# Kernel tuning notes

Measured on AMD Instinct MI355X. Metric: run time of the kernel, lower is better.

## Reference

```python
import jax
jax.config.update("jax_enable_x64", True)
import jax.numpy as jnp
import numpy as np
import math

B, L = 4, 4096
VOCAB, CVOCAB = 32000, 25000
HIDDEN, EDIM, NHEADS = 1024, 64, 8
NGRAMS = (2, 3)
TABLE_HINT = 100003
KSIZE, DILATION = 4, 3  # dilation = max ngram order
EPS = 1e-6


def _next_prime(n):
    if n <= 2:
        return 2
    c = n if n % 2 else n + 1
    while True:
        if all(c % i for i in range(3, int(math.isqrt(c)) + 1, 2)):
            return c
        c += 2


def _table_sizes():
    sizes, cur = [], TABLE_HINT
    for _ in range(NHEADS):
        p = _next_prime(cur)
        sizes.append(p)
        cur = p + 2
    return sizes


def setup_inputs():
    key = jax.random.key(0)
    ks = jax.random.split(key, 12)
    sizes = _table_sizes()  # identical for both ngram orders (same hint)
    max_s = max(sizes)
    n_orders = NGRAMS[1] - NGRAMS[0] + 1  # 2
    table_sizes = jnp.asarray(np.tile(np.array(sizes, dtype=np.int64), (n_orders, 1)))  # [2,8]
    tables = 0.01 * jax.random.normal(ks[0], (n_orders, NHEADS, max_s, EDIM), dtype=jnp.float32)
    return {
        "hidden_states": jax.random.normal(ks[1], (B, L, HIDDEN), dtype=jnp.float32),
        "token_ids": jax.random.randint(ks[2], (B, L), 0, VOCAB, dtype=jnp.int64),
        "projection": jax.random.randint(ks[3], (VOCAB,), 0, CVOCAB, dtype=jnp.int64),
        "mults2": jax.random.randint(ks[4], (NHEADS, 2), 1, 2**31 - 1, dtype=jnp.int64),
        "mults3": jax.random.randint(ks[5], (NHEADS, 3), 1, 2**31 - 1, dtype=jnp.int64),
        "table_sizes": table_sizes,
        "tables": tables,
        "w_k": (jax.random.normal(ks[6], (HIDDEN, n_orders * NHEADS * EDIM), dtype=jnp.float32) / math.sqrt(n_orders * NHEADS * EDIM)),
        "w_v": (jax.random.normal(ks[7], (HIDDEN, n_orders * NHEADS * EDIM), dtype=jnp.float32) / math.sqrt(n_orders * NHEADS * EDIM)),
        "q_norm_w": jnp.ones((HIDDEN,), dtype=jnp.float32),
        "k_norm_w": jnp.ones((HIDDEN,), dtype=jnp.float32),
        "conv_norm_w": jnp.ones((HIDDEN,), dtype=jnp.float32),
        "conv_w": 0.02 * jax.random.normal(ks[8], (HIDDEN, KSIZE), dtype=jnp.float32),
        "conv_b": jnp.zeros((HIDDEN,), dtype=jnp.float32),
    }


def _rmsnorm(x, w):
    norm = jax.lax.rsqrt(jnp.mean(jnp.square(x.astype(jnp.float32)), axis=-1, keepdims=True) + EPS)
    return (x.astype(jnp.float32) * norm).astype(x.dtype) * w


def _build_ngrams(compressed, n):
    # compressed: [B,L] int64 -> [B,L,n] causal windows with left zero pad
    p = jnp.pad(compressed, ((0, 0), (n - 1, 0)))
    return jnp.stack([p[:, i:i + compressed.shape[1]] for i in range(n)], axis=-1)


def _hash(ngrams, mults, sizes):
    # ngrams [B,L,n], mults [H,n], sizes [H] -> [B,L,H]
    prod = ngrams[:, :, None, :] * mults[None, None, :, :]  # int64
    mix = prod[..., 0]
    for i in range(1, prod.shape[-1]):
        mix = mix ^ prod[..., i]
    return jnp.abs(mix) % sizes[None, None, :]


def reference(hidden_states, token_ids, projection, mults2, mults3, table_sizes,
              tables, w_k, w_v, q_norm_w, k_norm_w, conv_norm_w, conv_w, conv_b):
    b, l, hidden = hidden_states.shape
    # ---- retrieve ----
    compressed = projection[jnp.clip(token_ids, 0, projection.shape[0] - 1)]  # [B,L]
    idx2 = _hash(_build_ngrams(compressed, 2), mults2, table_sizes[0])  # [B,L,H]
    idx3 = _hash(_build_ngrams(compressed, 3), mults3, table_sizes[1])  # [B,L,H]
    idx = jnp.concatenate([idx2, idx3], axis=-1)  # [B,L,2H] order: ngram2 heads, ngram3 heads
    n_tab = tables.shape[0] * tables.shape[1]
    tab_flat = tables.reshape(n_tab, tables.shape[2], tables.shape[3])
    emb = tab_flat[jnp.arange(n_tab), idx]  # [B,L,2H,EDIM] gather
    memory = emb.reshape(b, l, -1)  # [B,L,total_retrieval_dim]
    # ---- fuse ----
    k = jnp.einsum('bld,hd->blh', memory, w_k)
    v = jnp.einsum('bld,hd->blh', memory, w_v)
    q_n = _rmsnorm(hidden_states, q_norm_w)
    k_n = _rmsnorm(k, k_norm_w)
    scale = 1.0 / math.sqrt(hidden)
    gate = jax.nn.sigmoid(jnp.sum(q_n * k_n, axis=-1, keepdims=True) * scale)
    v_g = gate * v
    # ---- short conv (causal depthwise, dilation=3, kernel=4) ----
    h = _rmsnorm(v_g, conv_norm_w)
    pad = (KSIZE - 1) * DILATION  # 9; right padding is sliced off by [..., :L]
    hp = jnp.pad(h, ((0, 0), (pad, 0), (0, 0)))
    y = conv_b
    for j in range(KSIZE):
        y = y + hp[:, j * DILATION: j * DILATION + l, :] * conv_w[None, None, :, j]
    return jax.nn.silu(y) + v_g


if __name__ == "__main__":
    out = reference(**setup_inputs())
    print(out.shape, out.dtype)
```

## Files before the change

kernel.cpp:

```cpp
#include <hip/hip_runtime.h>
#include <hip/hip_bf16.h>
#include <math.h>

typedef unsigned short u16;
typedef __bf16 bf16x8 __attribute__((ext_vector_type(8)));
typedef float f32x4 __attribute__((ext_vector_type(4)));
typedef unsigned short u16x4 __attribute__((ext_vector_type(4)));
typedef unsigned short u16x8 __attribute__((ext_vector_type(8)));

#define BB 4
#define LL 4096
#define MTOK (BB*LL)
#define HID 1024
#define NKV 2048
#define KDIM 1024
#define VOCABN 32000
#define EPSF 1e-6f

__device__ __forceinline__ float bf2f(u16 x) {
  unsigned u = ((unsigned)x) << 16;
  return __builtin_bit_cast(float, u);
}
__device__ __forceinline__ u16 f2bf(float f) {
  unsigned u = __builtin_bit_cast(unsigned, f);
  u += 0x7FFFu + ((u >> 16) & 1u);
  return (u16)(u >> 16);
}

__global__ __launch_bounds__(256) void k_gather_conv(
    const int* __restrict__ tok, const int* __restrict__ proj,
    const int* __restrict__ m2, const int* __restrict__ m3,
    const int* __restrict__ tsz, const float* __restrict__ tables,
    int max_s, u16* __restrict__ mem,
    const float* __restrict__ wk, const float* __restrict__ wv,
    u16* __restrict__ W) {
  const int blk = blockIdx.x;
  const int tid = threadIdx.x;
  if (blk >= MTOK / 16) {
    int i = (blk - MTOK / 16) * 256 + tid;
    const int n4 = (NKV * KDIM) / 4;
    const int half = n4 / 2;
    const f32x4* src = (i < half) ? (const f32x4*)wk : (const f32x4*)wv;
    int j = (i < half) ? i : i - half;
    f32x4 v = src[j];
    u16x4 o = { f2bf(v[0]), f2bf(v[1]), f2bf(v[2]), f2bf(v[3]) };
    *(u16x4*)&W[(size_t)i * 4] = o;
    return;
  }
  __shared__ int sidx[16][16];
  const int m0 = blk * 16;
  const int tt = tid >> 4;
  const int t = tid & 15;
  const int m = m0 + tt;
  const int l = m & (LL - 1);

  long long c0, c1 = 0, c2 = 0;
  {
    int tk = tok[m];
    tk = tk < 0 ? 0 : (tk > VOCABN - 1 ? VOCABN - 1 : tk);
    c0 = proj[tk];
  }
  if (l >= 1) {
    int tk = tok[m - 1];
    tk = tk < 0 ? 0 : (tk > VOCABN - 1 ? VOCABN - 1 : tk);
    c1 = proj[tk];
  }
  if (l >= 2) {
    int tk = tok[m - 2];
    tk = tk < 0 ? 0 : (tk > VOCABN - 1 ? VOCABN - 1 : tk);
    c2 = proj[tk];
  }
  int order = t >> 3, h = t & 7;
  long long mix;
  if (order == 0) {
    mix = (c1 * (long long)m2[h * 2 + 0]) ^ (c0 * (long long)m2[h * 2 + 1]);
  } else {
    mix = (c2 * (long long)m3[h * 3 + 0]) ^ (c1 * (long long)m3[h * 3 + 1]) ^
          (c0 * (long long)m3[h * 3 + 2]);
  }
  unsigned long long um = (unsigned long long)(mix < 0 ? -mix : mix);
  unsigned long long usz = (unsigned long long)tsz[t];
  unsigned long long qq = (unsigned long long)((double)um / (double)usz);
  long long r = (long long)(um - qq * usz);
  if (r < 0) r += (long long)usz;
  else if (r >= (long long)usz) r -= (long long)usz;
  sidx[tt][t] = (int)r;
  __syncthreads();

  const int q = t;
#pragma unroll
  for (int it = 0; it < 16; ++it) {
    int idx = sidx[tt][it];
    const f32x4* src = (const f32x4*)(tables + ((size_t)it * (size_t)max_s + (size_t)idx) * 64);
    f32x4 e = src[q];
    u16x4 o = { f2bf(e[0]), f2bf(e[1]), f2bf(e[2]), f2bf(e[3]) };
    *(u16x4*)&mem[(size_t)m * HID + it * 64 + q * 4] = o;
  }
}

#define GBK2 32
#define BUF2 32768

__device__ __forceinline__ void gload16(const void* g, void* l) {
  __builtin_amdgcn_global_load_lds((__attribute__((address_space(1))) void*)(g),
                                   (__attribute__((address_space(3))) void*)(l), 16, 0, 0);
}
__device__ __forceinline__ int swz32(int x) { return x ^ (((x >> 6) & 3) << 4); }

__global__ __launch_bounds__(512, 2) void k_gemm(const u16* __restrict__ A,
                                                 const u16* __restrict__ Bw,
                                                 u16* __restrict__ C) {
  __shared__ __align__(16) char lds[131072];
  const int d = blockIdx.x;
  const int wg = (d & 7) * 64 + (d >> 3);
  const int bm = wg >> 3, bn = wg & 7;
  const int tid = threadIdx.x;
  const int w = tid >> 6, lane = tid & 63;
  const int wm = w >> 2, wn = w & 3;
  const int lm = lane & 15, kg = lane >> 4;

  const int ca0 = w * 2, ca1 = w * 2 + 1;
  const int row0 = ca0 * 16 + (lane >> 2);
  const int row1 = ca1 * 16 + (lane >> 2);
  const int off0 = row0 * KDIM + (((lane & 3) ^ (row0 & 3)) << 3);
  const int off1 = row1 * KDIM + (((lane & 3) ^ (row1 & 3)) << 3);
  const int dstA0 = ca0 * 1024 + lane * 16;
  const int dstA1 = ca1 * 1024 + lane * 16;
  const u16* Ap = A + (size_t)bm * 256 * KDIM;
  const u16* Bp = Bw + (size_t)bn * 256 * KDIM;

  int aro[8], bro[4];
#pragma unroll
  for (int mi = 0; mi < 8; ++mi)
    aro[mi] = swz32((wm * 128 + mi * 16 + lm) * 64 + kg * 16);
#pragma unroll
  for (int ni = 0; ni < 4; ++ni)
    bro[ni] = 16384 + swz32((wn * 64 + ni * 16 + lm) * 64 + kg * 16);

  f32x4 acc[8][4];
#pragma unroll
  for (int i = 0; i < 8; ++i)
#pragma unroll
    for (int j = 0; j < 4; ++j) acc[i][j] = (f32x4){0.f, 0.f, 0.f, 0.f};

#define STGA(kt, bb)                                                       \
  {                                                                        \
    char* bbase = lds + (bb) * BUF2;                                       \
    gload16(Ap + off0 + (kt) * GBK2, bbase + dstA0);                       \
    gload16(Ap + off1 + (kt) * GBK2, bbase + dstA1);                       \
  }
#define STGB(kt, bb)                                                       \
  {                                                                        \
    char* bbase = lds + (bb) * BUF2;                                       \
    gload16(Bp + off0 + (kt) * GBK2, bbase + 16384 + dstA0);               \
    gload16(Bp + off1 + (kt) * GBK2, bbase + 16384 + dstA1);               \
  }

#define TILE(t, bb, VMS, DOSTG)                                            \
  {                                                                        \
    asm volatile("s_waitcnt vmcnt(" VMS ")" ::: "memory");                 \
    __builtin_amdgcn_s_barrier();                                          \
    const char* buf = lds + (bb) * BUF2;                                   \
    bf16x8 af0[4], bfr[4], af1[4];                                         \
    _Pragma("unroll")                                                      \
    for (int mi = 0; mi < 4; ++mi) af0[mi] = *(const bf16x8*)(buf + aro[mi]); \
    _Pragma("unroll")                                                      \
    for (int ni = 0; ni < 4; ++ni) bfr[ni] = *(const bf16x8*)(buf + bro[ni]); \
    if (DOSTG) STGA((t) + 3, ((bb) + 3) & 3);                              \
    _Pragma("unroll")                                                      \
    for (int mi = 0; mi < 4; ++mi) af1[mi] = *(const bf16x8*)(buf + aro[4 + mi]); \
    if (DOSTG) STGB((t) + 3, ((bb) + 3) & 3);                              \
    __builtin_amdgcn_sched_barrier(0);                                     \
    asm volatile("s_waitcnt lgkmcnt(4)" ::: "memory");                     \
    __builtin_amdgcn_sched_barrier(0);                                     \
    __builtin_amdgcn_s_setprio(1);                                         \
    _Pragma("unroll")                                                      \
    for (int mi = 0; mi < 4; ++mi)                                         \
      _Pragma("unroll")                                                    \
      for (int ni = 0; ni < 4; ++ni)                                       \
        acc[mi][ni] = __builtin_amdgcn_mfma_f32_16x16x32_bf16(af0[mi], bfr[ni], acc[mi][ni], 0, 0, 0); \
    __builtin_amdgcn_s_setprio(0);                                         \
    __builtin_amdgcn_sched_barrier(0);                                     \
    asm volatile("s_waitcnt lgkmcnt(0)" ::: "memory");                     \
    __builtin_amdgcn_sched_barrier(0);                                     \
    __builtin_amdgcn_s_setprio(1);                                         \
    _Pragma("unroll")                                                      \
    for (int mi = 0; mi < 4; ++mi)                                         \
      _Pragma("unroll")                                                    \
      for (int ni = 0; ni < 4; ++ni)                                       \
        acc[4 + mi][ni] = __builtin_amdgcn_mfma_f32_16x16x32_bf16(af1[mi], bfr[ni], acc[4 + mi][ni], 0, 0, 0); \
    __builtin_amdgcn_s_setprio(0);                                         \
  }

  STGA(0, 0); STGB(0, 0);
  STGA(1, 1); STGB(1, 1);
  STGA(2, 2); STGB(2, 2);
#pragma unroll 1
  for (int t4 = 0; t4 < 7; ++t4) {
    const int t = t4 * 4;
    TILE(t + 0, 0, "8", 1);
    TILE(t + 1, 1, "8", 1);
    TILE(t + 2, 2, "8", 1);
    TILE(t + 3, 3, "8", 1);
  }
  TILE(28, 0, "8", 1);
  TILE(29, 1, "8", 0);
  TILE(30, 2, "4", 0);
  TILE(31, 3, "0", 0);
#undef STGA
#undef STGB
#undef TILE

  __syncthreads();
  u16* tile = (u16*)lds;
#pragma unroll
  for (int mi = 0; mi < 8; ++mi)
#pragma unroll
    for (int ni = 0; ni < 4; ++ni)
#pragma unroll
      for (int jj = 0; jj < 4; ++jj) {
        int r = wm * 128 + mi * 16 + kg * 4 + jj;
        int ccol = wn * 64 + ni * 16 + lm;
        tile[r * 256 + ccol] = f2bf(acc[mi][ni][jj]);
      }
  __syncthreads();
#pragma unroll
  for (int it = 0; it < 8; ++it) {
    int r = it * 32 + (tid >> 4);
    int cb = (tid & 15) * 32;
    *(f32x4*)((char*)C + ((size_t)(bm * 256 + r) * NKV + bn * 256) * 2 + cb) =
        *(const f32x4*)((char*)tile + r * 512 + cb);
    *(f32x4*)((char*)C + ((size_t)(bm * 256 + r) * NKV + bn * 256) * 2 + cb + 16) =
        *(const f32x4*)((char*)tile + r * 512 + cb + 16);
  }
}

#define CR 32

__global__ __launch_bounds__(256, 2) void k_gateconv(
    const float* __restrict__ hidden, const u16* __restrict__ KV,
    const float* __restrict__ qw, const float* __restrict__ kw,
    const float* __restrict__ cw, const float* __restrict__ convw,
    const float* __restrict__ convb, float* __restrict__ out) {
  __shared__ u16 ring[32][1024];
  const int blk = blockIdx.x;
  const int b = blk >> 7;
  const int l0 = (blk & 127) * CR;
  const int w = threadIdx.x >> 6, ln = threadIdx.x & 63;

  float qk[16], cwv[16];
  f32x4 wt[16];
  f32x4 cbv[4];
#pragma unroll
  for (int seg = 0; seg < 2; ++seg) {
    int c0 = seg * 512 + ln * 8;
    f32x4 qa = *(const f32x4*)&qw[c0], qb = *(const f32x4*)&qw[c0 + 4];
    f32x4 ka = *(const f32x4*)&kw[c0], kb = *(const f32x4*)&kw[c0 + 4];
    f32x4 ca = *(const f32x4*)&cw[c0], cbx = *(const f32x4*)&cw[c0 + 4];
#pragma unroll
    for (int i = 0; i < 4; ++i) {
      qk[seg * 8 + i] = qa[i] * ka[i];
      qk[seg * 8 + 4 + i] = qb[i] * kb[i];
      cwv[seg * 8 + i] = ca[i];
      cwv[seg * 8 + 4 + i] = cbx[i];
    }
    cbv[seg * 2] = *(const f32x4*)&convb[c0];
    cbv[seg * 2 + 1] = *(const f32x4*)&convb[c0 + 4];
#pragma unroll
    for (int e = 0; e < 8; ++e) wt[seg * 8 + e] = *(const f32x4*)&convw[(c0 + e) * 4];
  }

  const int base = l0 - 12;
  f32x4 x0, x1, x2, x3, nx0, nx1, nx2, nx3;
  u16x8 kk0, kk1, vv0, vv1, nk0, nk1, nv0, nv1;

#define LOADROW(r, X0, X1, X2, X3, K0, K1, V0, V1)                             \
  {                                                                            \
    X0 = (f32x4){0.f,0.f,0.f,0.f}; X1 = X0; X2 = X0; X3 = X0;                  \
    K0 = (u16x8){0,0,0,0,0,0,0,0}; K1 = K0; V0 = K0; V1 = K0;                  \
    if ((r) >= l0 - 9 && (r) >= 0) {                                           \
      size_t mr = (size_t)b * LL + (r);                                        \
      X0 = *(const f32x4*)&hidden[mr * HID + ln * 8];                          \
      X1 = *(const f32x4*)&hidden[mr * HID + ln * 8 + 4];                      \
      X2 = *(const f32x4*)&hidden[mr * HID + 512 + ln * 8];                    \
      X3 = *(const f32x4*)&hidden[mr * HID + 512 + ln * 8 + 4];                \
      K0 = *(const u16x8*)&KV[mr * NKV + ln * 8];                              \
      K1 = *(const u16x8*)&KV[mr * NKV + 512 + ln * 8];                        \
      V0 = *(const u16x8*)&KV[mr * NKV + HID + ln * 8];                        \
      V1 = *(const u16x8*)&KV[mr * NKV + HID + 512 + ln * 8];                  \
    }                                                                          \
  }

  LOADROW(base + w, x0, x1, x2, x3, kk0, kk1, vv0, vv1);

#pragma unroll 1
  for (int g = 0; g < 11; ++g) {
    const int r = base + g * 4 + w;
    if (g < 10) {
      LOADROW(r + 4, nx0, nx1, nx2, nx3, nk0, nk1, nv0, nv1);
    }
    float s0 = 0.f, s1 = 0.f, s2 = 0.f, s3 = 0.f;
#pragma unroll
    for (int e = 0; e < 8; ++e) {
      float xa = (e < 4) ? x0[e] : x1[e - 4];
      float xb = (e < 4) ? x2[e] : x3[e - 4];
      float ka = bf2f(kk0[e]), kb = bf2f(kk1[e]);
      float va = bf2f(vv0[e]), vb = bf2f(vv1[e]);
      s0 += xa * xa + xb * xb;
      s1 += ka * ka + kb * kb;
      s2 += xa * qk[e] * ka + xb * qk[8 + e] * kb;
      s3 += va * va + vb * vb;
    }
#pragma unroll
    for (int mm = 32; mm >= 1; mm >>= 1) {
      s0 += __shfl_xor(s0, mm, 64);
      s1 += __shfl_xor(s1, mm, 64);
      s2 += __shfl_xor(s2, mm, 64);
      s3 += __shfl_xor(s3, mm, 64);
    }
    const float inv = 0.0009765625f;
    float rq = rsqrtf(s0 * inv + EPSF);
    float rk = rsqrtf(s1 * inv + EPSF);
    float gate = 1.f / (1.f + expf(-rq * rk * s2 * 0.03125f));
    float rv = rsqrtf(gate * gate * s3 * inv + EPSF);
    float grv = gate * rv;

    u16x8 h0p, h1p;
#pragma unroll
    for (int e = 0; e < 8; ++e) {
      h0p[e] = f2bf(bf2f(vv0[e]) * grv * cwv[e]);
      h1p[e] = f2bf(bf2f(vv1[e]) * grv * cwv[8 + e]);
    }
    const int slot = r & 31;
    *(u16x8*)&ring[slot][ln * 8] = h0p;
    *(u16x8*)&ring[slot][512 + ln * 8] = h1p;
    __syncthreads();

    if (r >= l0) {
      const int s9 = (r - 9) & 31, s6 = (r - 6) & 31, s3s = (r - 3) & 31;
      size_t mr = (size_t)b * LL + r;
#pragma unroll
      for (int seg = 0; seg < 2; ++seg) {
        u16x8 a9 = *(const u16x8*)&ring[s9][seg * 512 + ln * 8];
        u16x8 a6 = *(const u16x8*)&ring[s6][seg * 512 + ln * 8];
        u16x8 a3 = *(const u16x8*)&ring[s3s][seg * 512 + ln * 8];
        const u16x8 vv = seg ? vv1 : vv0;
        f32x4 ra, rb;
#pragma unroll
        for (int e = 0; e < 8; ++e) {
          const int idx = seg * 8 + e;
          float vf = bf2f(vv[e]);
          float hown = vf * grv * cwv[idx];
          f32x4 wv = wt[idx];
          float y = cbv[seg * 2 + (e >> 2)][e & 3] + bf2f(a9[e]) * wv[0] +
                    bf2f(a6[e]) * wv[1] + bf2f(a3[e]) * wv[2] + hown * wv[3];
          float res = y / (1.f + expf(-y)) + gate * vf;
          if (e < 4) ra[e] = res; else rb[e - 4] = res;
        }
        *(f32x4*)&out[mr * HID + seg * 512 + ln * 8] = ra;
        *(f32x4*)&out[mr * HID + seg * 512 + ln * 8 + 4] = rb;
      }
    }
    x0 = nx0; x1 = nx1; x2 = nx2; x3 = nx3;
    kk0 = nk0; kk1 = nk1; vv0 = nv0; vv1 = nv1;
  }
#undef LOADROW
}

extern "C" void kernel_launch(void* const* d_in, const int* in_sizes, int n_in,
                              void* d_out, int out_size, void* d_ws, size_t ws_size,
                              hipStream_t stream) {
  const float* hidden   = (const float*)d_in[0];
  const int*   tok      = (const int*)d_in[1];
  const int*   proj     = (const int*)d_in[2];
  const int*   m2       = (const int*)d_in[3];
  const int*   m3       = (const int*)d_in[4];
  const int*   tsz      = (const int*)d_in[5];
  const float* tables   = (const float*)d_in[6];
  const float* wk       = (const float*)d_in[7];
  const float* wv       = (const float*)d_in[8];
  const float* qw       = (const float*)d_in[9];
  const float* kw       = (const float*)d_in[10];
  const float* cnw      = (const float*)d_in[11];
  const float* convw    = (const float*)d_in[12];
  const float* convb    = (const float*)d_in[13];
  float* out = (float*)d_out;

  const int max_s = in_sizes[6] / (2 * 8 * 64);

  char* ws = (char*)d_ws;
  u16* mem = (u16*)ws;
  u16* W   = (u16*)(ws + (size_t)33554432);
  u16* KV  = (u16*)(ws + (size_t)33554432 + 4194304);

  k_gather_conv<<<dim3(MTOK / 16 + (NKV * KDIM / 4) / 256), dim3(256), 0, stream>>>(
      tok, proj, m2, m3, tsz, tables, max_s, mem, wk, wv, W);
  k_gemm<<<dim3((MTOK / 256) * (NKV / 256)), dim3(512), 0, stream>>>(mem, W, KV);
  k_gateconv<<<dim3(BB * (LL / CR)), dim3(256), 0, stream>>>(hidden, KV, qw, kw, cnw, convw, convb, out);
}
```

Baseline: 146.4 us.

## Fuse gate reductions into GEMM epilogue and drop K from global memory

The GEMM epilogue now computes per-row partial sums (hidden squares, k squares, q·k dot, v squares) for each 256-column tile and writes them as small float arrays. Only V is stored to global memory, and K is no longer written at all. The gate/conv kernel reads these partials instead of hidden and K, which removes the large hidden-state and K traffic and the wave-wide shuffle reductions there. The cost is extra work in the GEMM epilogue, where it re-reads hidden rows, which could unbalance the K-tile blocks against the V-tile blocks. The conv kernel also uses a smaller ring buffer and 16 contiguous channels per lane.

```diff
diff --git a/kernel.cpp b/kernel.cpp
--- a/kernel.cpp
+++ b/kernel.cpp
@@ -12,7 +12,6 @@
 #define LL 4096
 #define MTOK (BB*LL)
 #define HID 1024
-#define NKV 2048
 #define KDIM 1024
 #define VOCABN 32000
 #define EPSF 1e-6f
@@ -38,7 +37,7 @@
   const int tid = threadIdx.x;
   if (blk >= MTOK / 16) {
     int i = (blk - MTOK / 16) * 256 + tid;
-    const int n4 = (NKV * KDIM) / 4;
+    const int n4 = (2048 * KDIM) / 4;
     const int half = n4 / 2;
     const f32x4* src = (i < half) ? (const f32x4*)wk : (const f32x4*)wv;
     int j = (i < half) ? i : i - half;
@@ -107,9 +106,12 @@
 }
 __device__ __forceinline__ int swz32(int x) { return x ^ (((x >> 6) & 3) << 4); }
 
-__global__ __launch_bounds__(512, 2) void k_gemm(const u16* __restrict__ A,
-                                                 const u16* __restrict__ Bw,
-                                                 u16* __restrict__ C) {
+__global__ __launch_bounds__(512, 2) void k_gemm(
+    const u16* __restrict__ A, const u16* __restrict__ Bw,
+    const float* __restrict__ hidden, const float* __restrict__ qw,
+    const float* __restrict__ kw, u16* __restrict__ Cv,
+    float* __restrict__ kp0, float* __restrict__ kp1,
+    float* __restrict__ kp2, float* __restrict__ kp3) {
   __shared__ __align__(16) char lds[131072];
   const int d = blockIdx.x;
   const int wg = (d & 7) * 64 + (d >> 3);
@@ -224,99 +226,114 @@
         tile[r * 256 + ccol] = f2bf(acc[mi][ni][jj]);
       }
   __syncthreads();
-#pragma unroll
-  for (int it = 0; it < 8; ++it) {
-    int r = it * 32 + (tid >> 4);
-    int cb = (tid & 15) * 32;
-    *(f32x4*)((char*)C + ((size_t)(bm * 256 + r) * NKV + bn * 256) * 2 + cb) =
-        *(const f32x4*)((char*)tile + r * 512 + cb);
-    *(f32x4*)((char*)C + ((size_t)(bm * 256 + r) * NKV + bn * 256) * 2 + cb + 16) =
-        *(const f32x4*)((char*)tile + r * 512 + cb + 16);
+
+  const int row2 = tid >> 1;
+  const int ch = (tid & 1) * 128;
+  const int grow = bm * 256 + row2;
+  if (bn < 4) {
+    const float* hrow = hidden + (size_t)grow * HID + bn * 256 + ch;
+    const float* qp = qw + bn * 256 + ch;
+    const float* kp_ = kw + bn * 256 + ch;
+    float s0 = 0.f, s1 = 0.f, s2 = 0.f;
+#pragma unroll 4
+    for (int j = 0; j < 128; j += 4) {
+      f32x4 xv = *(const f32x4*)&hrow[j];
+      f32x4 qv = *(const f32x4*)&qp[j];
+      f32x4 kv = *(const f32x4*)&kp_[j];
+      u16x4 kk = *(const u16x4*)&tile[row2 * 256 + ch + j];
+#pragma unroll
+      for (int i = 0; i < 4; ++i) {
+        float kf = bf2f(kk[i]);
+        s0 += xv[i] * xv[i];
+        s1 += kf * kf;
+        s2 += xv[i] * qv[i] * kv[i] * kf;
+      }
+    }
+    s0 += __shfl_xor(s0, 1, 64);
+    s1 += __shfl_xor(s1, 1, 64);
+    s2 += __shfl_xor(s2, 1, 64);
+    if ((tid & 1) == 0) {
+      kp0[bn * MTOK + grow] = s0;
+      kp1[bn * MTOK + grow] = s1;
+      kp2[bn * MTOK + grow] = s2;
+    }
+  } else {
+#pragma unroll
+    for (int it = 0; it < 8; ++it) {
+      int r = it * 32 + (tid >> 4);
+      int cb = (tid & 15) * 32;
+      *(f32x4*)((char*)Cv + ((size_t)(bm * 256 + r) * 1024 + (bn - 4) * 256) * 2 + cb) =
+          *(const f32x4*)((char*)tile + r * 512 + cb);
+      *(f32x4*)((char*)Cv + ((size_t)(bm * 256 + r) * 1024 + (bn - 4) * 256) * 2 + cb + 16) =
+          *(const f32x4*)((char*)tile + r * 512 + cb + 16);
+    }
+    float s3 = 0.f;
+#pragma unroll 4
+    for (int j = 0; j < 128; j += 4) {
+      u16x4 vv4 = *(const u16x4*)&tile[row2 * 256 + ch + j];
+#pragma unroll
+      for (int i = 0; i < 4; ++i) {
+        float vf = bf2f(vv4[i]);
+        s3 += vf * vf;
+      }
+    }
+    s3 += __shfl_xor(s3, 1, 64);
+    if ((tid & 1) == 0) kp3[(bn - 4) * MTOK + grow] = s3;
   }
 }
 
 #define CR 32
 
-__global__ __launch_bounds__(256, 2) void k_gateconv(
-    const float* __restrict__ hidden, const u16* __restrict__ KV,
-    const float* __restrict__ qw, const float* __restrict__ kw,
-    const float* __restrict__ cw, const float* __restrict__ convw,
-    const float* __restrict__ convb, float* __restrict__ out) {
-  __shared__ u16 ring[32][1024];
+__global__ __launch_bounds__(256) void k_gateconv(
+    const u16* __restrict__ Vv, const float* __restrict__ kp0,
+    const float* __restrict__ kp1, const float* __restrict__ kp2,
+    const float* __restrict__ kp3, const float* __restrict__ cw,
+    const float* __restrict__ convw, const float* __restrict__ convb,
+    float* __restrict__ out) {
+  __shared__ u16 ring[16][1024];
   const int blk = blockIdx.x;
   const int b = blk >> 7;
   const int l0 = (blk & 127) * CR;
   const int w = threadIdx.x >> 6, ln = threadIdx.x & 63;
-
-  float qk[16], cwv[16];
+  const int c0 = ln * 16;
+
+  float cwv[16], cbv[16];
   f32x4 wt[16];
-  f32x4 cbv[4];
-#pragma unroll
-  for (int seg = 0; seg < 2; ++seg) {
-    int c0 = seg * 512 + ln * 8;
-    f32x4 qa = *(const f32x4*)&qw[c0], qb = *(const f32x4*)&qw[c0 + 4];
-    f32x4 ka = *(const f32x4*)&kw[c0], kb = *(const f32x4*)&kw[c0 + 4];
-    f32x4 ca = *(const f32x4*)&cw[c0], cbx = *(const f32x4*)&cw[c0 + 4];
-#pragma unroll
-    for (int i = 0; i < 4; ++i) {
-      qk[seg * 8 + i] = qa[i] * ka[i];
-      qk[seg * 8 + 4 + i] = qb[i] * kb[i];
-      cwv[seg * 8 + i] = ca[i];
-      cwv[seg * 8 + 4 + i] = cbx[i];
-    }
-    cbv[seg * 2] = *(const f32x4*)&convb[c0];
-    cbv[seg * 2 + 1] = *(const f32x4*)&convb[c0 + 4];
-#pragma unroll
-    for (int e = 0; e < 8; ++e) wt[seg * 8 + e] = *(const f32x4*)&convw[(c0 + e) * 4];
-  }
+#pragma unroll
+  for (int e = 0; e < 16; e += 4) {
+    *(f32x4*)&cwv[e] = *(const f32x4*)&cw[c0 + e];
+    *(f32x4*)&cbv[e] = *(const f32x4*)&convb[c0 + e];
+  }
+#pragma unroll
+  for (int e = 0; e < 16; ++e) wt[e] = *(const f32x4*)&convw[(c0 + e) * 4];
 
   const int base = l0 - 12;
-  f32x4 x0, x1, x2, x3, nx0, nx1, nx2, nx3;
-  u16x8 kk0, kk1, vv0, vv1, nk0, nk1, nv0, nv1;
-
-#define LOADROW(r, X0, X1, X2, X3, K0, K1, V0, V1)                             \
-  {                                                                            \
-    X0 = (f32x4){0.f,0.f,0.f,0.f}; X1 = X0; X2 = X0; X3 = X0;                  \
-    K0 = (u16x8){0,0,0,0,0,0,0,0}; K1 = K0; V0 = K0; V1 = K0;                  \
-    if ((r) >= l0 - 9 && (r) >= 0) {                                           \
-      size_t mr = (size_t)b * LL + (r);                                        \
-      X0 = *(const f32x4*)&hidden[mr * HID + ln * 8];                          \
-      X1 = *(const f32x4*)&hidden[mr * HID + ln * 8 + 4];                      \
-      X2 = *(const f32x4*)&hidden[mr * HID + 512 + ln * 8];                    \
-      X3 = *(const f32x4*)&hidden[mr * HID + 512 + ln * 8 + 4];                \
-      K0 = *(const u16x8*)&KV[mr * NKV + ln * 8];                              \
-      K1 = *(const u16x8*)&KV[mr * NKV + 512 + ln * 8];                        \
-      V0 = *(const u16x8*)&KV[mr * NKV + HID + ln * 8];                        \
-      V1 = *(const u16x8*)&KV[mr * NKV + HID + 512 + ln * 8];                  \
-    }                                                                          \
-  }
-
-  LOADROW(base + w, x0, x1, x2, x3, kk0, kk1, vv0, vv1);
+  u16x8 v0, v1, nv0, nv1;
+
+#define LOADV(r, V0, V1)                                                     \
+  {                                                                          \
+    V0 = (u16x8){0,0,0,0,0,0,0,0}; V1 = V0;                                  \
+    if ((r) >= 0) {                                                          \
+      size_t mr_ = (size_t)b * LL + (r);                                     \
+      V0 = *(const u16x8*)&Vv[mr_ * 1024 + c0];                              \
+      V1 = *(const u16x8*)&Vv[mr_ * 1024 + c0 + 8];                          \
+    }                                                                        \
+  }
+
+  LOADV(base + w, v0, v1);
 
 #pragma unroll 1
   for (int g = 0; g < 11; ++g) {
     const int r = base + g * 4 + w;
-    if (g < 10) {
-      LOADROW(r + 4, nx0, nx1, nx2, nx3, nk0, nk1, nv0, nv1);
-    }
+    if (g < 10) { LOADV(r + 4, nv0, nv1); }
+
     float s0 = 0.f, s1 = 0.f, s2 = 0.f, s3 = 0.f;
-#pragma unroll
-    for (int e = 0; e < 8; ++e) {
-      float xa = (e < 4) ? x0[e] : x1[e - 4];
-      float xb = (e < 4) ? x2[e] : x3[e - 4];
-      float ka = bf2f(kk0[e]), kb = bf2f(kk1[e]);
-      float va = bf2f(vv0[e]), vb = bf2f(vv1[e]);
-      s0 += xa * xa + xb * xb;
-      s1 += ka * ka + kb * kb;
-      s2 += xa * qk[e] * ka + xb * qk[8 + e] * kb;
-      s3 += va * va + vb * vb;
-    }
-#pragma unroll
-    for (int mm = 32; mm >= 1; mm >>= 1) {
-      s0 += __shfl_xor(s0, mm, 64);
-      s1 += __shfl_xor(s1, mm, 64);
-      s2 += __shfl_xor(s2, mm, 64);
-      s3 += __shfl_xor(s3, mm, 64);
+    if (r >= 0) {
+      const int mr = b * LL + r;
+      s0 = kp0[mr] + kp0[MTOK + mr] + kp0[2 * MTOK + mr] + kp0[3 * MTOK + mr];
+      s1 = kp1[mr] + kp1[MTOK + mr] + kp1[2 * MTOK + mr] + kp1[3 * MTOK + mr];
+      s2 = kp2[mr] + kp2[MTOK + mr] + kp2[2 * MTOK + mr] + kp2[3 * MTOK + mr];
+      s3 = kp3[mr] + kp3[MTOK + mr] + kp3[2 * MTOK + mr] + kp3[3 * MTOK + mr];
     }
     const float inv = 0.0009765625f;
     float rq = rsqrtf(s0 * inv + EPSF);
@@ -325,46 +342,44 @@
     float rv = rsqrtf(gate * gate * s3 * inv + EPSF);
     float grv = gate * rv;
 
+    float hf[16];
     u16x8 h0p, h1p;
 #pragma unroll
     for (int e = 0; e < 8; ++e) {
-      h0p[e] = f2bf(bf2f(vv0[e]) * grv * cwv[e]);
-      h1p[e] = f2bf(bf2f(vv1[e]) * grv * cwv[8 + e]);
-    }
-    const int slot = r & 31;
-    *(u16x8*)&ring[slot][ln * 8] = h0p;
-    *(u16x8*)&ring[slot][512 + ln * 8] = h1p;
+      hf[e] = bf2f(v0[e]) * grv * cwv[e];
+      hf[8 + e] = bf2f(v1[e]) * grv * cwv[8 + e];
+      h0p[e] = f2bf(hf[e]);
+      h1p[e] = f2bf(hf[8 + e]);
+    }
+    const int slot = r & 15;
+    *(u16x8*)&ring[slot][c0] = h0p;
+    *(u16x8*)&ring[slot][c0 + 8] = h1p;
     __syncthreads();
 
     if (r >= l0) {
-      const int s9 = (r - 9) & 31, s6 = (r - 6) & 31, s3s = (r - 3) & 31;
-      size_t mr = (size_t)b * LL + r;
-#pragma unroll
-      for (int seg = 0; seg < 2; ++seg) {
-        u16x8 a9 = *(const u16x8*)&ring[s9][seg * 512 + ln * 8];
-        u16x8 a6 = *(const u16x8*)&ring[s6][seg * 512 + ln * 8];
-        u16x8 a3 = *(const u16x8*)&ring[s3s][seg * 512 + ln * 8];
-        const u16x8 vv = seg ? vv1 : vv0;
-        f32x4 ra, rb;
-#pragma unroll
-        for (int e = 0; e < 8; ++e) {
-          const int idx = seg * 8 + e;
-          float vf = bf2f(vv[e]);
-          float hown = vf * grv * cwv[idx];
-          f32x4 wv = wt[idx];
-          float y = cbv[seg * 2 + (e >> 2)][e & 3] + bf2f(a9[e]) * wv[0] +
-                    bf2f(a6[e]) * wv[1] + bf2f(a3[e]) * wv[2] + hown * wv[3];
-          float res = y / (1.f + expf(-y)) + gate * vf;
-          if (e < 4) ra[e] = res; else rb[e - 4] = res;
-        }
-        *(f32x4*)&out[mr * HID + seg * 512 + ln * 8] = ra;
-        *(f32x4*)&out[mr * HID + seg * 512 + ln * 8 + 4] = rb;
+      const int s9 = (r - 9) & 15, s6 = (r - 6) & 15, s3s = (r - 3) & 15;
+      const size_t mr = (size_t)b * LL + r;
+      u16x8 a9l = *(const u16x8*)&ring[s9][c0],  a9h = *(const u16x8*)&ring[s9][c0 + 8];
+      u16x8 a6l = *(const u16x8*)&ring[s6][c0],  a6h = *(const u16x8*)&ring[s6][c0 + 8];
+      u16x8 a3l = *(const u16x8*)&ring[s3s][c0], a3h = *(const u16x8*)&ring[s3s][c0 + 8];
+      f32x4 res[4];
+#pragma unroll
+      for (int e = 0; e < 16; ++e) {
+        float vf = (e < 8) ? bf2f(v0[e & 7]) : bf2f(v1[e & 7]);
+        float t9 = (e < 8) ? bf2f(a9l[e & 7]) : bf2f(a9h[e & 7]);
+        float t6 = (e < 8) ? bf2f(a6l[e & 7]) : bf2f(a6h[e & 7]);
+        float t3 = (e < 8) ? bf2f(a3l[e & 7]) : bf2f(a3h[e & 7]);
+        f32x4 wv = wt[e];
+        float y = cbv[e] + t9 * wv[0] + t6 * wv[1] + t3 * wv[2] + hf[e] * wv[3];
+        res[e >> 2][e & 3] = y / (1.f + expf(-y)) + gate * vf;
       }
-    }
-    x0 = nx0; x1 = nx1; x2 = nx2; x3 = nx3;
-    kk0 = nk0; kk1 = nk1; vv0 = nv0; vv1 = nv1;
-  }
-#undef LOADROW
+#pragma unroll
+      for (int j = 0; j < 4; ++j)
+        *(f32x4*)&out[mr * HID + c0 + j * 4] = res[j];
+    }
+    v0 = nv0; v1 = nv1;
+  }
+#undef LOADV
 }
 
 extern "C" void kernel_launch(void* const* d_in, const int* in_sizes, int n_in,
@@ -389,12 +404,18 @@
   const int max_s = in_sizes[6] / (2 * 8 * 64);
 
   char* ws = (char*)d_ws;
-  u16* mem = (u16*)ws;
-  u16* W   = (u16*)(ws + (size_t)33554432);
-  u16* KV  = (u16*)(ws + (size_t)33554432 + 4194304);
-
-  k_gather_conv<<<dim3(MTOK / 16 + (NKV * KDIM / 4) / 256), dim3(256), 0, stream>>>(
+  u16*   mem = (u16*)ws;
+  u16*   W   = (u16*)(ws + (size_t)33554432);
+  u16*   Cv  = (u16*)(ws + (size_t)37748736);
+  float* kp0 = (float*)(ws + (size_t)71303168);
+  float* kp1 = (float*)(ws + (size_t)71565312);
+  float* kp2 = (float*)(ws + (size_t)71827456);
+  float* kp3 = (float*)(ws + (size_t)72089600);
+
+  k_gather_conv<<<dim3(MTOK / 16 + (2048 * KDIM / 4) / 256), dim3(256), 0, stream>>>(
       tok, proj, m2, m3, tsz, tables, max_s, mem, wk, wv, W);
-  k_gemm<<<dim3((MTOK / 256) * (NKV / 256)), dim3(512), 0, stream>>>(mem, W, KV);
-  k_gateconv<<<dim3(BB * (LL / CR)), dim3(256), 0, stream>>>(hidden, KV, qw, kw, cnw, convw, convb, out);
-}
+  k_gemm<<<dim3((MTOK / 256) * 8), dim3(512), 0, stream>>>(
+      mem, W, hidden, qw, kw, Cv, kp0, kp1, kp2, kp3);
+  k_gateconv<<<dim3(BB * (LL / CR)), dim3(256), 0, stream>>>(
+      Cv, kp0, kp1, kp2, kp3, cnw, convw, convb, out);
+}
```

After: 158.1 us. 8.0% more time.
